# Kernel optimization log

Measured on AMD Instinct MI355X. Metric: run time of the kernel, lower is better.

## Reference

```python
import jax, jax.numpy as jnp
import numpy as np
import math

B, L, DM, H, TD, K = 4, 1024, 1024, 16, 8, 8
D = DM // H  # head_dim = 64


def setup_inputs() -> dict:
    key = jax.random.key(0)
    ks = jax.random.split(key, 20)
    shape = (H, D, TD, K)
    inp = {
        'P': jax.random.normal(ks[0], (B, L, DM), jnp.float32),
        't': jax.random.uniform(ks[1], (B, L, TD), jnp.float32),
    }
    i = 2
    for nm in ('Q', 'K', 'V'):
        inp['mu_' + nm] = jax.random.normal(ks[i], shape, jnp.float32); i += 1
        inp['sigma_' + nm] = jnp.clip(jnp.abs(jax.random.normal(ks[i], shape, jnp.float32)), 0.001); i += 1
        inp['w_' + nm] = jax.random.normal(ks[i], shape, jnp.float32); i += 1
        inp['gamma_' + nm] = jnp.zeros((H, D), jnp.float32)
        inp['W_' + nm] = jax.random.normal(ks[i], (H, D, D), jnp.float32); i += 1
    inp['W_O_w'] = jax.random.normal(ks[i], (DM, DM), jnp.float32) * (1.0 / math.sqrt(DM)); i += 1
    inp['W_O_b'] = jnp.zeros((DM,), jnp.float32)
    return inp


def _gaussian_kernel(t, mu, sigma, w):
    # t: [B,L,T]; mu/sigma/w: [H,D,T,K] -> out [B,L,H,D]
    tt = t[:, :, None, None, :, None]              # [B,L,1,1,T,1]
    g = w * jnp.exp(-(tt - mu) ** 2 / (2.0 * sigma ** 2))  # [B,L,H,D,T,K]
    return g.sum(axis=(-1, -2))


def reference(P, t, mu_Q, sigma_Q, w_Q, gamma_Q, W_Q,
              mu_K, sigma_K, w_K, gamma_K, W_K,
              mu_V, sigma_V, w_V, gamma_V, W_V,
              W_O_w, W_O_b):
    Bv, Lv, _ = P.shape
    Ph = P.reshape(Bv, Lv, H, D)                    # [B,L,H,D]
    Q = _gaussian_kernel(t, mu_Q, sigma_Q, w_Q) * Ph + gamma_Q
    Kx = _gaussian_kernel(t, mu_K, sigma_K, w_K) * Ph + gamma_K
    V = _gaussian_kernel(t, mu_V, sigma_V, w_V) * Ph + gamma_V
    Q = jnp.einsum('blhd,hdf->blhf', Q, W_Q)
    Kx = jnp.einsum('blhd,hdf->blhf', Kx, W_K)
    V = jnp.einsum('blhd,hdf->blhf', V, W_V)
    scores = jnp.einsum('blhf,bmhf->bhlm', Q, Kx) / math.sqrt(D)
    A = jax.nn.softmax(scores, axis=-1)
    out = jnp.einsum('bhlm,bmhf->blhf', A, V).reshape(Bv, Lv, DM)
    return out @ W_O_w.T + W_O_b
```

## Files before the change

kernel.cpp:

```cpp
#include <hip/hip_runtime.h>
#include <cstdint>

#define DEVI __device__ __forceinline__

constexpr int Bc = 4, Lc = 1024, DMc = 1024, Hc = 16, TDc = 8, Kc = 8, Dc = 64;
constexpr int NBL = Bc * Lc;
constexpr int PAR = Hc * Dc * TDc * Kc;

using f16x8 = __attribute__((ext_vector_type(8))) _Float16;
using f16x4 = __attribute__((ext_vector_type(4))) _Float16;
using s16x8 = __attribute__((ext_vector_type(8))) short;
using s16x4 = __attribute__((ext_vector_type(4))) short;
using f32x4 = __attribute__((ext_vector_type(4))) float;
using f32x2 = __attribute__((ext_vector_type(2))) float;

DEVI unsigned short f2bf(float x){
  union { float f; unsigned u; } v; v.f = x;
  return (unsigned short)((v.u + 0x7fffu + ((v.u >> 16) & 1u)) >> 16);
}

DEVI unsigned cvtpk_bf16(float lo, float hi){
  unsigned r;
  asm("v_cvt_pk_bf16_f32 %0, %1, %2" : "=v"(r) : "v"(lo), "v"(hi));
  return r;
}

#define SWZ_ON 1
DEVI int swz(int row, int unit){
#if SWZ_ON
  return unit ^ (row & 7);
#else
  (void)row; return unit;
#endif
}

__global__ __launch_bounds__(256) void k0_pack(
    const float* __restrict__ muQ, const float* __restrict__ sgQ, const float* __restrict__ wQ, const float* __restrict__ gQ,
    const float* __restrict__ muK, const float* __restrict__ sgK, const float* __restrict__ wK, const float* __restrict__ gK,
    const float* __restrict__ muV, const float* __restrict__ sgV, const float* __restrict__ wV, const float* __restrict__ gV,
    float* __restrict__ PK, float* __restrict__ GA)
{
  const float c = 0.8493218002880191f;
  const int i = blockIdx.x * 256 + threadIdx.x;
  if (i < 3 * PAR){
    const int p = i / PAR, j = i - p * PAR;
    const float* mu = (p == 0) ? muQ : (p == 1) ? muK : muV;
    const float* sg = (p == 0) ? sgQ : (p == 1) ? sgK : sgV;
    const float* w  = (p == 0) ? wQ  : (p == 1) ? wK  : wV;
    PK[((size_t)p * 3 + 0) * PAR + j] = mu[j];
    PK[((size_t)p * 3 + 1) * PAR + j] = c / sg[j];
    PK[((size_t)p * 3 + 2) * PAR + j] = w[j];
  }
  if (i < 3 * Hc * 64){
    const int p = i / (Hc * 64), j = i - p * (Hc * 64);
    const float* g = (p == 0) ? gQ : (p == 1) ? gK : gV;
    GA[i] = g[j];
  }
}

__global__ __launch_bounds__(256) void k0_wo(const float* __restrict__ WO, unsigned short* __restrict__ WOb)
{
  int i = blockIdx.x * 256 + threadIdx.x;
  if (i < DMc * DMc) WOb[i] = f2bf(WO[i]);
}

__global__ __launch_bounds__(256) void k0_wsplit(
    const float* __restrict__ WQ, const float* __restrict__ WK, const float* __restrict__ WV,
    _Float16* __restrict__ Whi, _Float16* __restrict__ Wlo)
{
  int i = blockIdx.x * 256 + threadIdx.x;
  if (i >= 3 * Hc * 64 * 64) return;
  const int d = i & 63, f = (i >> 6) & 63, h = (i >> 12) & 15, p = i >> 16;
  const float* W = (p == 0) ? WQ : (p == 1) ? WK : WV;
  float v = W[((size_t)h * 64 + d) * 64 + f];
  if (p == 0) v *= 0.18033688011112042f;
  const _Float16 hi = (_Float16)v;
  Whi[i] = hi;
  Wlo[i] = (_Float16)(v - (float)hi);
}

__global__ __launch_bounds__(256) void k1_gauss(
    const float* __restrict__ P, const float* __restrict__ t,
    const float* __restrict__ PK, const float* __restrict__ GA,
    float* __restrict__ OG)
{
  __shared__ float gbuf[64 * 65];
  const int h = blockIdx.x, tile = blockIdx.y, p = blockIdx.z;
  const int tid = threadIdx.x, lane = tid & 63;
  const int wv = __builtin_amdgcn_readfirstlane(tid >> 6);
  const int bl0 = tile * 64;

  const float* mu = PK + ((size_t)p * 3 + 0) * PAR;
  const float* al = PK + ((size_t)p * 3 + 1) * PAR;
  const float* wp = PK + ((size_t)p * 3 + 2) * PAR;
  const float* gm = GA + p * (Hc * 64);
  float*       op = OG + (size_t)p * NBL * DMc;

  float tv[8];
  {
    const float4 t0 = *(const float4*)&t[(size_t)(bl0 + lane) * 8];
    const float4 t1 = *(const float4*)&t[(size_t)(bl0 + lane) * 8 + 4];
    tv[0] = t0.x; tv[1] = t0.y; tv[2] = t0.z; tv[3] = t0.w;
    tv[4] = t1.x; tv[5] = t1.y; tv[6] = t1.z; tv[7] = t1.w;
  }

  #pragma unroll 2
  for (int dd = 0; dd < 16; ++dd){
    const int d = wv * 16 + dd;
    const int base = (h * 64 + d) * 64;
    f32x2 g01 = {0.f, 0.f}, g23 = {0.f, 0.f};
    #pragma unroll
    for (int td = 0; td < 8; ++td){
      const float tval = tv[td];
      const f32x2 tt2 = {tval, tval};
      #pragma unroll
      for (int kk = 0; kk < 4; ++kk){
        const int idx = base + td * 8 + kk * 2;
        const f32x2 m2 = *(const f32x2*)&mu[idx];
        const f32x2 a2 = *(const f32x2*)&al[idx];
        const f32x2 w2 = *(const f32x2*)&wp[idx];
        const f32x2 u  = (tt2 - m2) * a2;
        const f32x2 nu = u * u;
        f32x2 e;
        e[0] = __builtin_amdgcn_exp2f(-nu[0]);
        e[1] = __builtin_amdgcn_exp2f(-nu[1]);
        if (kk & 1) g23 += w2 * e;
        else        g01 += w2 * e;
      }
    }
    gbuf[d * 65 + lane] = (g01[0] + g01[1]) + (g23[0] + g23[1]);
  }
  __syncthreads();

  {
    const int dl = tid & 63, rq = tid >> 6;
    const float gam = gm[h * 64 + dl];
    #pragma unroll 4
    for (int rr = 0; rr < 16; ++rr){
      const int r = rq * 16 + rr;
      const float g  = gbuf[dl * 65 + r];
      const float ph = P[(size_t)(bl0 + r) * DMc + h * 64 + dl];
      op[(size_t)(bl0 + r) * DMc + h * 64 + dl] = fmaf(g, ph, gam);
    }
  }
}

__global__ __launch_bounds__(256) void k2m(
    const float* __restrict__ Qg, const float* __restrict__ Kg, const float* __restrict__ Vg,
    const _Float16* __restrict__ Wsp_hi, const _Float16* __restrict__ Wsp_lo,
    _Float16* __restrict__ Qhi, _Float16* __restrict__ Qlo,
    _Float16* __restrict__ Khi, _Float16* __restrict__ Klo,
    unsigned short* __restrict__ Vt)
{
  __shared__ __align__(16) _Float16 XhiL[64 * 64];
  __shared__ __align__(16) _Float16 XloL[64 * 64];
  __shared__ __align__(16) _Float16 WhiL[64 * 64];
  __shared__ __align__(16) _Float16 WloL[64 * 64];
  const int h = blockIdx.x, tile = blockIdx.y, p = blockIdx.z;
  const int tid = threadIdx.x, lane = tid & 63, wv = tid >> 6;
  const int lrow = lane & 15, lgrp = lane >> 4;
  const int bl0 = tile * 64;

  const float* Xg = (p == 0) ? Qg : (p == 1) ? Kg : Vg;

  for (int i = tid; i < 1024; i += 256){
    const int row = i >> 4, c4 = i & 15;
    const float4 x = *(const float4*)&Xg[(size_t)(bl0 + row) * DMc + h * 64 + c4 * 4];
    const float xs[4] = {x.x, x.y, x.z, x.w};
    f16x4 hx, lx;
    #pragma unroll
    for (int j = 0; j < 4; ++j){
      hx[j] = (_Float16)xs[j];
      lx[j] = (_Float16)(xs[j] - (float)hx[j]);
    }
    const int off = row * 128 + swz(row, c4 >> 1) * 16 + (c4 & 1) * 8;
    *(f16x4*)((char*)XhiL + off) = hx;
    *(f16x4*)((char*)XloL + off) = lx;
  }
  {
    const _Float16* wh = Wsp_hi + ((size_t)p * Hc + h) * 4096;
    const _Float16* wl = Wsp_lo + ((size_t)p * Hc + h) * 4096;
    for (int i = tid; i < 512; i += 256){
      const int f = i >> 3, u = i & 7;
      *(f16x8*)((char*)WhiL + f * 128 + swz(f, u) * 16) = *(const f16x8*)(wh + f * 64 + u * 8);
      *(f16x8*)((char*)WloL + f * 128 + swz(f, u) * 16) = *(const f16x8*)(wl + f * 64 + u * 8);
    }
  }
  __syncthreads();

  f32x4 acc[4] = {};
  if (p < 2){
    #pragma unroll
    for (int ks = 0; ks < 2; ++ks){
      const int arow = wv * 16 + lrow;
      const int aoff = arow * 128 + swz(arow, ks * 4 + lgrp) * 16;
      f16x8 xh = *(const f16x8*)((const char*)XhiL + aoff);
      f16x8 xl = *(const f16x8*)((const char*)XloL + aoff);
      #pragma unroll
      for (int tf = 0; tf < 4; ++tf){
        const int brow = tf * 16 + lrow;
        const int boff = brow * 128 + swz(brow, ks * 4 + lgrp) * 16;
        f16x8 wh_ = *(const f16x8*)((const char*)WhiL + boff);
        f16x8 wl_ = *(const f16x8*)((const char*)WloL + boff);
        acc[tf] = __builtin_amdgcn_mfma_f32_16x16x32_f16(xh, wh_, acc[tf], 0, 0, 0);
        acc[tf] = __builtin_amdgcn_mfma_f32_16x16x32_f16(xl, wh_, acc[tf], 0, 0, 0);
        acc[tf] = __builtin_amdgcn_mfma_f32_16x16x32_f16(xh, wl_, acc[tf], 0, 0, 0);
      }
    }
  } else {
    #pragma unroll
    for (int ks = 0; ks < 2; ++ks){
      const int arow = wv * 16 + lrow;
      const int aoff = arow * 128 + swz(arow, ks * 4 + lgrp) * 16;
      f16x8 wh_ = *(const f16x8*)((const char*)WhiL + aoff);
      f16x8 wl_ = *(const f16x8*)((const char*)WloL + aoff);
      #pragma unroll
      for (int mt = 0; mt < 4; ++mt){
        const int brow = mt * 16 + lrow;
        const int boff = brow * 128 + swz(brow, ks * 4 + lgrp) * 16;
        f16x8 xh = *(const f16x8*)((const char*)XhiL + boff);
        f16x8 xl = *(const f16x8*)((const char*)XloL + boff);
        acc[mt] = __builtin_amdgcn_mfma_f32_16x16x32_f16(wh_, xh, acc[mt], 0, 0, 0);
        acc[mt] = __builtin_amdgcn_mfma_f32_16x16x32_f16(wl_, xh, acc[mt], 0, 0, 0);
        acc[mt] = __builtin_amdgcn_mfma_f32_16x16x32_f16(wh_, xl, acc[mt], 0, 0, 0);
      }
    }
  }

  const int b = bl0 >> 10, l0 = bl0 & 1023;
  if (p == 0){
    #pragma unroll
    for (int tf = 0; tf < 4; ++tf){
      const int f = tf * 16 + lrow;
      #pragma unroll
      for (int r = 0; r < 4; ++r){
        const int l = l0 + wv * 16 + lgrp * 4 + r;
        const float a = acc[tf][r];
        const _Float16 hi = (_Float16)a;
        const _Float16 lo = (_Float16)(a - (float)hi);
        const size_t o = (((size_t)b * Hc + h) * Lc + l) * 64 + f;
        Qhi[o] = hi; Qlo[o] = lo;
      }
    }
  } else if (p == 1){
    #pragma unroll
    for (int tf = 0; tf < 4; ++tf){
      const int f = tf * 16 + lrow;
      #pragma unroll
      for (int r = 0; r < 4; ++r){
        const int l = l0 + wv * 16 + lgrp * 4 + r;
        const float a = acc[tf][r];
        const _Float16 hi = (_Float16)a;
        const _Float16 lo = (_Float16)(a - (float)hi);
        const size_t o = (((size_t)b * Hc + h) * Lc + l) * 64 + (swz(l, f >> 3) << 3) + (f & 7);
        Khi[o] = hi; Klo[o] = lo;
      }
    }
  } else {
    const size_t basev = (((size_t)b * Hc + h) * 64) * Lc + l0;
    #pragma unroll
    for (int mt = 0; mt < 4; ++mt){
      const int ml = mt * 16 + lrow;
      #pragma unroll
      for (int r = 0; r < 4; ++r){
        const int f = wv * 16 + lgrp * 4 + r;
        Vt[basev + (size_t)f * Lc + (swz(f, ml >> 3) << 3) + (ml & 7)] = f2bf(acc[mt][r]);
      }
    }
  }
}

__global__ __launch_bounds__(256) void k3_attn(
    const _Float16* __restrict__ Qhi, const _Float16* __restrict__ Qlo,
    const _Float16* __restrict__ Khi, const _Float16* __restrict__ Klo,
    const unsigned short* __restrict__ Vt,
    unsigned short* __restrict__ AO)
{
  __shared__ __align__(16) _Float16 KhiL[64 * 64];
  __shared__ __align__(16) _Float16 KloL[64 * 64];
  __shared__ __align__(16) unsigned short VL[64 * 64];
  __shared__ __align__(16) unsigned short PL[4][16 * 64];
  const int bh = blockIdx.x, qt = blockIdx.y;
  const int tid = threadIdx.x, wv = tid >> 6, lane = tid & 63;
  const int lrow = lane & 15, lgrp = lane >> 4;
  const size_t bhL = (size_t)bh * Lc;

  f16x8 qh[2], ql[2];
  {
    const int qrow = qt * 64 + wv * 16 + lrow;
    const _Float16* q1 = &Qhi[(bhL + qrow) * 64 + lgrp * 8];
    const _Float16* q2 = &Qlo[(bhL + qrow) * 64 + lgrp * 8];
    qh[0] = *(const f16x8*)q1; qh[1] = *(const f16x8*)(q1 + 32);
    ql[0] = *(const f16x8*)q2; ql[1] = *(const f16x8*)(q2 + 32);
  }

  f32x4 o[4] = {};
  float mrun = -1e30f, lrun = 0.f;

  const int i0 = tid, i1 = tid + 256;
  const char* kbase = (const char*)(Khi + bhL * 64);
  const char* lbase = (const char*)(Klo + bhL * 64);
  const char* vbase = (const char*)(Vt + (size_t)bh * 64 * Lc);
  const int voff0 = (i0 >> 3) * 2048 + (i0 & 7) * 16;
  const int voff1 = (i1 >> 3) * 2048 + (i1 & 7) * 16;

  f16x8 ra0 = *(const f16x8*)(kbase + i0 * 16);
  f16x8 ra1 = *(const f16x8*)(kbase + i1 * 16);
  f16x8 rb0 = *(const f16x8*)(lbase + i0 * 16);
  f16x8 rb1 = *(const f16x8*)(lbase + i1 * 16);
  s16x8 rc0 = *(const s16x8*)(vbase + voff0);
  s16x8 rc1 = *(const s16x8*)(vbase + voff1);

  #pragma unroll 1
  for (int kt = 0; kt < 16; ++kt){
    __syncthreads();
    *(f16x8*)((char*)KhiL + i0 * 16) = ra0;
    *(f16x8*)((char*)KhiL + i1 * 16) = ra1;
    *(f16x8*)((char*)KloL + i0 * 16) = rb0;
    *(f16x8*)((char*)KloL + i1 * 16) = rb1;
    *(s16x8*)((char*)VL + i0 * 16) = rc0;
    *(s16x8*)((char*)VL + i1 * 16) = rc1;
    if (kt + 1 < 16){
      const char* kn = kbase + (kt + 1) * 8192;
      const char* ln = lbase + (kt + 1) * 8192;
      const char* vn = vbase + (kt + 1) * 128;
      ra0 = *(const f16x8*)(kn + i0 * 16);
      ra1 = *(const f16x8*)(kn + i1 * 16);
      rb0 = *(const f16x8*)(ln + i0 * 16);
      rb1 = *(const f16x8*)(ln + i1 * 16);
      rc0 = *(const s16x8*)(vn + voff0);
      rc1 = *(const s16x8*)(vn + voff1);
    }
    __syncthreads();

    f32x4 s[4] = {};
    #pragma unroll
    for (int tt = 0; tt < 4; ++tt){
      #pragma unroll
      for (int ks = 0; ks < 2; ++ks){
        const int m = tt * 16 + lrow;
        const int off = m * 128 + swz(m, ks * 4 + lgrp) * 16;
        f16x8 kh_ = *(const f16x8*)((const char*)KhiL + off);
        f16x8 kl_ = *(const f16x8*)((const char*)KloL + off);
        s[tt] = __builtin_amdgcn_mfma_f32_16x16x32_f16(kh_, qh[ks], s[tt], 0, 0, 0);
        s[tt] = __builtin_amdgcn_mfma_f32_16x16x32_f16(kh_, ql[ks], s[tt], 0, 0, 0);
        s[tt] = __builtin_amdgcn_mfma_f32_16x16x32_f16(kl_, qh[ks], s[tt], 0, 0, 0);
      }
    }

    float v;
    {
      float v0 = fmaxf(fmaxf(s[0][0], s[0][1]), fmaxf(s[0][2], s[0][3]));
      float v1 = fmaxf(fmaxf(s[1][0], s[1][1]), fmaxf(s[1][2], s[1][3]));
      float v2 = fmaxf(fmaxf(s[2][0], s[2][1]), fmaxf(s[2][2], s[2][3]));
      float v3 = fmaxf(fmaxf(s[3][0], s[3][1]), fmaxf(s[3][2], s[3][3]));
      v = fmaxf(fmaxf(v0, v1), fmaxf(v2, v3));
      v = fmaxf(v, __shfl_xor(v, 16));
      v = fmaxf(v, __shfl_xor(v, 32));
    }
    const float mn = fmaxf(mrun, v);
    const float sc = __builtin_amdgcn_exp2f(mrun - mn);
    mrun = mn;

    float rs = 0.f;
    float pp[4][4];
    #pragma unroll
    for (int tt = 0; tt < 4; ++tt){
      #pragma unroll
      for (int r = 0; r < 4; ++r){
        const float p = __builtin_amdgcn_exp2f(s[tt][r] - mn);
        rs += p;
        pp[tt][r] = p;
      }
    }
    rs += __shfl_xor(rs, 16);
    rs += __shfl_xor(rs, 32);
    lrun = lrun * sc + rs;
    #pragma unroll
    for (int t2 = 0; t2 < 4; ++t2){
      o[t2][0] *= sc; o[t2][1] *= sc; o[t2][2] *= sc; o[t2][3] *= sc;
    }

    short* pw = (short*)PL[wv];
    #pragma unroll
    for (int tt = 0; tt < 4; ++tt){
      uint2 pk;
      pk.x = cvtpk_bf16(pp[tt][0], pp[tt][1]);
      pk.y = cvtpk_bf16(pp[tt][2], pp[tt][3]);
      const int off = lrow * 128 + swz(lrow, tt * 2 + (lgrp >> 1)) * 16 + (lgrp & 1) * 8;
      *(uint2*)((char*)pw + off) = pk;
    }
    asm volatile("s_waitcnt lgkmcnt(0)" ::: "memory");
    __builtin_amdgcn_sched_barrier(0);

    #pragma unroll
    for (int ks = 0; ks < 2; ++ks){
      const int poff = lrow * 128 + swz(lrow, ks * 4 + lgrp) * 16;
      s16x8 pa = *(const s16x8*)((const char*)pw + poff);
      #pragma unroll
      for (int t2 = 0; t2 < 4; ++t2){
        const int f = t2 * 16 + lrow;
        const int voff = f * 128 + swz(f, ks * 4 + lgrp) * 16;
        s16x8 vb = *(const s16x8*)((const char*)VL + voff);
        o[t2] = __builtin_amdgcn_mfma_f32_16x16x32_bf16(vb, pa, o[t2], 0, 0, 0);
      }
    }
  }

  const int b = bh >> 4, hh = bh & 15;
  const float inv = 1.0f / lrun;
  const int l = qt * 64 + wv * 16 + lrow;
  unsigned short* aorow = &AO[((size_t)(b * Lc + l)) * DMc + hh * 64];
  #pragma unroll
  for (int t2 = 0; t2 < 4; ++t2){
    uint2 ov;
    ov.x = cvtpk_bf16(o[t2][0] * inv, o[t2][1] * inv);
    ov.y = cvtpk_bf16(o[t2][2] * inv, o[t2][3] * inv);
    *(uint2*)(aorow + t2 * 16 + lgrp * 4) = ov;
  }
}

__global__ __launch_bounds__(256) void k4_out(
    const unsigned short* __restrict__ A, const unsigned short* __restrict__ Bw,
    const float* __restrict__ bias, float* __restrict__ out)
{
  __shared__ __align__(16) unsigned short Asl[128 * 64];
  __shared__ __align__(16) unsigned short Bsl[128 * 64];
  const int mt = blockIdx.x, nt = blockIdx.y;
  const int tid = threadIdx.x, wv = tid >> 6, lane = tid & 63;
  const int wr = wv >> 1, wc = wv & 1, lrow = lane & 15, lgrp = lane >> 4;
  f32x4 acc[4][4] = {};
  const char* abase = (const char*)A  + (size_t)mt * 128 * 2048;
  const char* bbase = (const char*)Bw + (size_t)nt * 128 * 2048;

  for (int kt = 0; kt < 16; ++kt){
    __syncthreads();
    #pragma unroll
    for (int q = 0; q < 4; ++q){
      const int i = q * 256 + tid, row = i >> 3, u = i & 7;
      s16x8 av = *(const s16x8*)(abase + (size_t)row * 2048 + kt * 128 + u * 16);
      s16x8 bv = *(const s16x8*)(bbase + (size_t)row * 2048 + kt * 128 + u * 16);
      *(s16x8*)((char*)Asl + row * 128 + swz(row, u) * 16) = av;
      *(s16x8*)((char*)Bsl + row * 128 + swz(row, u) * 16) = bv;
    }
    __syncthreads();
    #pragma unroll
    for (int ks = 0; ks < 2; ++ks){
      s16x8 af[4], bf[4];
      #pragma unroll
      for (int i4 = 0; i4 < 4; ++i4){
        const int row = wr * 64 + i4 * 16 + lrow;
        af[i4] = *(const s16x8*)((const char*)Asl + row * 128 + swz(row, ks * 4 + lgrp) * 16);
        const int col = wc * 64 + i4 * 16 + lrow;
        bf[i4] = *(const s16x8*)((const char*)Bsl + col * 128 + swz(col, ks * 4 + lgrp) * 16);
      }
      #pragma unroll
      for (int i4 = 0; i4 < 4; ++i4)
        #pragma unroll
        for (int j4 = 0; j4 < 4; ++j4)
          acc[i4][j4] = __builtin_amdgcn_mfma_f32_16x16x32_bf16(af[i4], bf[j4], acc[i4][j4], 0, 0, 0);
    }
  }
  #pragma unroll
  for (int i4 = 0; i4 < 4; ++i4)
    #pragma unroll
    for (int j4 = 0; j4 < 4; ++j4){
      const int col = nt * 128 + wc * 64 + j4 * 16 + lrow;
      const float bb = bias[col];
      #pragma unroll
      for (int r = 0; r < 4; ++r){
        const int row = mt * 128 + wr * 64 + i4 * 16 + lgrp * 4 + r;
        out[(size_t)row * DMc + col] = acc[i4][j4][r] + bb;
      }
    }
}

extern "C" void kernel_launch(void* const* d_in, const int* in_sizes, int n_in,
                              void* d_out, int out_size, void* d_ws, size_t ws_size,
                              hipStream_t stream)
{
  const float* P   = (const float*)d_in[0];
  const float* t   = (const float*)d_in[1];
  const float* muQ = (const float*)d_in[2];
  const float* sgQ = (const float*)d_in[3];
  const float* wQ  = (const float*)d_in[4];
  const float* gQ  = (const float*)d_in[5];
  const float* WQ  = (const float*)d_in[6];
  const float* muK = (const float*)d_in[7];
  const float* sgK = (const float*)d_in[8];
  const float* wK  = (const float*)d_in[9];
  const float* gK  = (const float*)d_in[10];
  const float* WK  = (const float*)d_in[11];
  const float* muV = (const float*)d_in[12];
  const float* sgV = (const float*)d_in[13];
  const float* wV  = (const float*)d_in[14];
  const float* gV  = (const float*)d_in[15];
  const float* WV  = (const float*)d_in[16];
  const float* WO  = (const float*)d_in[17];
  const float* WOb = (const float*)d_in[18];

  char* w = (char*)d_ws;
  auto take = [&](size_t bytes) -> char* {
    char* p = w; w += (bytes + 255) & ~(size_t)255; return p;
  };
  float* PKb = (float*)take((size_t)3 * 3 * PAR * 4);
  float* GAb = (float*)take((size_t)3 * Hc * 64 * 4);
  float* OG  = (float*)take((size_t)3 * NBL * DMc * 4);
  _Float16* Qhi = (_Float16*)take((size_t)NBL * DMc * 2);
  _Float16* Qlo = (_Float16*)take((size_t)NBL * DMc * 2);
  _Float16* Khi = (_Float16*)take((size_t)NBL * DMc * 2);
  _Float16* Klo = (_Float16*)take((size_t)NBL * DMc * 2);
  unsigned short* Vt    = (unsigned short*)take((size_t)NBL * DMc * 2);
  unsigned short* AO    = (unsigned short*)take((size_t)NBL * DMc * 2);
  unsigned short* WOb16 = (unsigned short*)take((size_t)DMc * DMc * 2);
  _Float16* Wsp_hi = (_Float16*)take((size_t)3 * Hc * 64 * 64 * 2);
  _Float16* Wsp_lo = (_Float16*)take((size_t)3 * Hc * 64 * 64 * 2);
  if ((size_t)(w - (char*)d_ws) > ws_size) return;

  float* Qg = OG;
  float* Kg = OG + (size_t)NBL * DMc;
  float* Vg = OG + (size_t)2 * NBL * DMc;

  k0_pack<<<(3 * PAR + 255) / 256, 256, 0, stream>>>(
      muQ, sgQ, wQ, gQ, muK, sgK, wK, gK, muV, sgV, wV, gV, PKb, GAb);
  k0_wo<<<DMc * DMc / 256, 256, 0, stream>>>(WO, WOb16);
  k0_wsplit<<<(3 * Hc * 64 * 64) / 256, 256, 0, stream>>>(WQ, WK, WV, Wsp_hi, Wsp_lo);
  k1_gauss<<<dim3(Hc, NBL / 64, 3), 256, 0, stream>>>(P, t, PKb, GAb, OG);
  k2m<<<dim3(Hc, NBL / 64, 3), 256, 0, stream>>>(Qg, Kg, Vg, Wsp_hi, Wsp_lo,
      Qhi, Qlo, Khi, Klo, Vt);
  k3_attn<<<dim3(Bc * Hc, Lc / 64), 256, 0, stream>>>(Qhi, Qlo, Khi, Klo, Vt, AO);
  k4_out<<<dim3(NBL / 128, DMc / 128), 256, 0, stream>>>(AO, WOb16, WOb, (float*)d_out);
}
```

Before: 204.6 us.

## Merge weight-prep kernels into one launch and enlarge attention blocks to 128 queries

Folds the three preprocessing kernels (parameter packing, W_O bf16 conversion, W_Q/K/V fp16 split) into a single launch, with block ranges picking the task, so two launch overheads go away. The attention kernel now runs 512 threads (8 waves) per block covering 128 query rows. Each K/V tile staged in shared memory is therefore reused by twice as many waves, and each thread loads one vector per tile instead of two. In exchange the attention grid has half as many blocks (512) and uses more shared memory per block, which can lower occupancy.

```diff
diff --git a/kernel.cpp b/kernel.cpp
--- a/kernel.cpp
+++ b/kernel.cpp
@@ -34,15 +34,23 @@
 #endif
 }
 
-__global__ __launch_bounds__(256) void k0_pack(
+__global__ __launch_bounds__(256) void k0_all(
     const float* __restrict__ muQ, const float* __restrict__ sgQ, const float* __restrict__ wQ, const float* __restrict__ gQ,
     const float* __restrict__ muK, const float* __restrict__ sgK, const float* __restrict__ wK, const float* __restrict__ gK,
     const float* __restrict__ muV, const float* __restrict__ sgV, const float* __restrict__ wV, const float* __restrict__ gV,
-    float* __restrict__ PK, float* __restrict__ GA)
+    const float* __restrict__ WQ, const float* __restrict__ WK, const float* __restrict__ WV,
+    const float* __restrict__ WO,
+    float* __restrict__ PK, float* __restrict__ GA,
+    _Float16* __restrict__ Whi, _Float16* __restrict__ Wlo,
+    unsigned short* __restrict__ WOb)
 {
-  const float c = 0.8493218002880191f;
-  const int i = blockIdx.x * 256 + threadIdx.x;
-  if (i < 3 * PAR){
+  const int bx = blockIdx.x;
+  if (bx < 4096){
+    const int i = bx * 256 + threadIdx.x;
+    WOb[i] = f2bf(WO[i]);
+  } else if (bx < 4096 + 768){
+    const float c = 0.8493218002880191f;
+    const int i = (bx - 4096) * 256 + threadIdx.x;
     const int p = i / PAR, j = i - p * PAR;
     const float* mu = (p == 0) ? muQ : (p == 1) ? muK : muV;
     const float* sg = (p == 0) ? sgQ : (p == 1) ? sgK : sgV;
@@ -50,33 +58,21 @@
     PK[((size_t)p * 3 + 0) * PAR + j] = mu[j];
     PK[((size_t)p * 3 + 1) * PAR + j] = c / sg[j];
     PK[((size_t)p * 3 + 2) * PAR + j] = w[j];
-  }
-  if (i < 3 * Hc * 64){
-    const int p = i / (Hc * 64), j = i - p * (Hc * 64);
-    const float* g = (p == 0) ? gQ : (p == 1) ? gK : gV;
-    GA[i] = g[j];
-  }
-}
-
-__global__ __launch_bounds__(256) void k0_wo(const float* __restrict__ WO, unsigned short* __restrict__ WOb)
-{
-  int i = blockIdx.x * 256 + threadIdx.x;
-  if (i < DMc * DMc) WOb[i] = f2bf(WO[i]);
-}
-
-__global__ __launch_bounds__(256) void k0_wsplit(
-    const float* __restrict__ WQ, const float* __restrict__ WK, const float* __restrict__ WV,
-    _Float16* __restrict__ Whi, _Float16* __restrict__ Wlo)
-{
-  int i = blockIdx.x * 256 + threadIdx.x;
-  if (i >= 3 * Hc * 64 * 64) return;
-  const int d = i & 63, f = (i >> 6) & 63, h = (i >> 12) & 15, p = i >> 16;
-  const float* W = (p == 0) ? WQ : (p == 1) ? WK : WV;
-  float v = W[((size_t)h * 64 + d) * 64 + f];
-  if (p == 0) v *= 0.18033688011112042f;
-  const _Float16 hi = (_Float16)v;
-  Whi[i] = hi;
-  Wlo[i] = (_Float16)(v - (float)hi);
+    if (i < 3 * Hc * 64){
+      const int pp = i / (Hc * 64), jj = i - pp * (Hc * 64);
+      const float* g = (pp == 0) ? gQ : (pp == 1) ? gK : gV;
+      GA[i] = g[jj];
+    }
+  } else {
+    const int i = (bx - 4096 - 768) * 256 + threadIdx.x;
+    const int d = i & 63, f = (i >> 6) & 63, h = (i >> 12) & 15, p = i >> 16;
+    const float* W = (p == 0) ? WQ : (p == 1) ? WK : WV;
+    float v = W[((size_t)h * 64 + d) * 64 + f];
+    if (p == 0) v *= 0.18033688011112042f;
+    const _Float16 hi = (_Float16)v;
+    Whi[i] = hi;
+    Wlo[i] = (_Float16)(v - (float)hi);
+  }
 }
 
 __global__ __launch_bounds__(256) void k1_gauss(
@@ -270,7 +266,7 @@
   }
 }
 
-__global__ __launch_bounds__(256) void k3_attn(
+__global__ __launch_bounds__(512) void k3_attn(
     const _Float16* __restrict__ Qhi, const _Float16* __restrict__ Qlo,
     const _Float16* __restrict__ Khi, const _Float16* __restrict__ Klo,
     const unsigned short* __restrict__ Vt,
@@ -279,7 +275,7 @@
   __shared__ __align__(16) _Float16 KhiL[64 * 64];
   __shared__ __align__(16) _Float16 KloL[64 * 64];
   __shared__ __align__(16) unsigned short VL[64 * 64];
-  __shared__ __align__(16) unsigned short PL[4][16 * 64];
+  __shared__ __align__(16) unsigned short PL[8][16 * 64];
   const int bh = blockIdx.x, qt = blockIdx.y;
   const int tid = threadIdx.x, wv = tid >> 6, lane = tid & 63;
   const int lrow = lane & 15, lgrp = lane >> 4;
@@ -287,7 +283,7 @@
 
   f16x8 qh[2], ql[2];
   {
-    const int qrow = qt * 64 + wv * 16 + lrow;
+    const int qrow = qt * 128 + wv * 16 + lrow;
     const _Float16* q1 = &Qhi[(bhL + qrow) * 64 + lgrp * 8];
     const _Float16* q2 = &Qlo[(bhL + qrow) * 64 + lgrp * 8];
     qh[0] = *(const f16x8*)q1; qh[1] = *(const f16x8*)(q1 + 32);
@@ -297,39 +293,28 @@
   f32x4 o[4] = {};
   float mrun = -1e30f, lrun = 0.f;
 
-  const int i0 = tid, i1 = tid + 256;
   const char* kbase = (const char*)(Khi + bhL * 64);
   const char* lbase = (const char*)(Klo + bhL * 64);
   const char* vbase = (const char*)(Vt + (size_t)bh * 64 * Lc);
-  const int voff0 = (i0 >> 3) * 2048 + (i0 & 7) * 16;
-  const int voff1 = (i1 >> 3) * 2048 + (i1 & 7) * 16;
-
-  f16x8 ra0 = *(const f16x8*)(kbase + i0 * 16);
-  f16x8 ra1 = *(const f16x8*)(kbase + i1 * 16);
-  f16x8 rb0 = *(const f16x8*)(lbase + i0 * 16);
-  f16x8 rb1 = *(const f16x8*)(lbase + i1 * 16);
+  const int voff0 = (tid >> 3) * 2048 + (tid & 7) * 16;
+
+  f16x8 ra0 = *(const f16x8*)(kbase + tid * 16);
+  f16x8 rb0 = *(const f16x8*)(lbase + tid * 16);
   s16x8 rc0 = *(const s16x8*)(vbase + voff0);
-  s16x8 rc1 = *(const s16x8*)(vbase + voff1);
 
   #pragma unroll 1
   for (int kt = 0; kt < 16; ++kt){
     __syncthreads();
-    *(f16x8*)((char*)KhiL + i0 * 16) = ra0;
-    *(f16x8*)((char*)KhiL + i1 * 16) = ra1;
-    *(f16x8*)((char*)KloL + i0 * 16) = rb0;
-    *(f16x8*)((char*)KloL + i1 * 16) = rb1;
-    *(s16x8*)((char*)VL + i0 * 16) = rc0;
-    *(s16x8*)((char*)VL + i1 * 16) = rc1;
+    *(f16x8*)((char*)KhiL + tid * 16) = ra0;
+    *(f16x8*)((char*)KloL + tid * 16) = rb0;
+    *(s16x8*)((char*)VL + tid * 16) = rc0;
     if (kt + 1 < 16){
       const char* kn = kbase + (kt + 1) * 8192;
       const char* ln = lbase + (kt + 1) * 8192;
       const char* vn = vbase + (kt + 1) * 128;
-      ra0 = *(const f16x8*)(kn + i0 * 16);
-      ra1 = *(const f16x8*)(kn + i1 * 16);
-      rb0 = *(const f16x8*)(ln + i0 * 16);
-      rb1 = *(const f16x8*)(ln + i1 * 16);
+      ra0 = *(const f16x8*)(kn + tid * 16);
+      rb0 = *(const f16x8*)(ln + tid * 16);
       rc0 = *(const s16x8*)(vn + voff0);
-      rc1 = *(const s16x8*)(vn + voff1);
     }
     __syncthreads();
 
@@ -409,7 +394,7 @@
 
   const int b = bh >> 4, hh = bh & 15;
   const float inv = 1.0f / lrun;
-  const int l = qt * 64 + wv * 16 + lrow;
+  const int l = qt * 128 + wv * 16 + lrow;
   unsigned short* aorow = &AO[((size_t)(b * Lc + l)) * DMc + hh * 64];
   #pragma unroll
   for (int t2 = 0; t2 < 4; ++t2){
@@ -521,13 +506,12 @@
   float* Kg = OG + (size_t)NBL * DMc;
   float* Vg = OG + (size_t)2 * NBL * DMc;
 
-  k0_pack<<<(3 * PAR + 255) / 256, 256, 0, stream>>>(
-      muQ, sgQ, wQ, gQ, muK, sgK, wK, gK, muV, sgV, wV, gV, PKb, GAb);
-  k0_wo<<<DMc * DMc / 256, 256, 0, stream>>>(WO, WOb16);
-  k0_wsplit<<<(3 * Hc * 64 * 64) / 256, 256, 0, stream>>>(WQ, WK, WV, Wsp_hi, Wsp_lo);
+  k0_all<<<4096 + 768 + 768, 256, 0, stream>>>(
+      muQ, sgQ, wQ, gQ, muK, sgK, wK, gK, muV, sgV, wV, gV,
+      WQ, WK, WV, WO, PKb, GAb, Wsp_hi, Wsp_lo, WOb16);
   k1_gauss<<<dim3(Hc, NBL / 64, 3), 256, 0, stream>>>(P, t, PKb, GAb, OG);
   k2m<<<dim3(Hc, NBL / 64, 3), 256, 0, stream>>>(Qg, Kg, Vg, Wsp_hi, Wsp_lo,
       Qhi, Qlo, Khi, Klo, Vt);
-  k3_attn<<<dim3(Bc * Hc, Lc / 64), 256, 0, stream>>>(Qhi, Qlo, Khi, Klo, Vt, AO);
+  k3_attn<<<dim3(Bc * Hc, Lc / 128), 512, 0, stream>>>(Qhi, Qlo, Khi, Klo, Vt, AO);
   k4_out<<<dim3(NBL / 128, DMc / 128), 256, 0, stream>>>(AO, WOb16, WOb, (float*)d_out);
 }
```

Result: faster. 191.0 us (median of 2 runs) (-6.6%).
